# Performance work log

Measured on AMD Instinct MI355X. Metric: run time of the kernel, lower is better.

The kernel has to match this reference:

```python
import jax, jax.numpy as jnp
import numpy as np

IN_CH, IN_DIM, OUT_CH, OUT_DIM = 16, 32, 32, 32
NUM_ITERS = 3
EPS = 1e-11


def setup_inputs() -> dict:
    key = jax.random.key(0)
    kx, kw = jax.random.split(key)
    B, N = 32, 128
    x = jax.random.normal(kx, (B, N, IN_CH, IN_DIM), dtype=jnp.float32)
    # learned transform, matches torch Parameter randn(1,1,in_ch,out_ch,in_dim,out_dim)
    W = jax.random.normal(kw, (IN_CH, OUT_CH, IN_DIM, OUT_DIM), dtype=jnp.float32)
    return {"x": x, "W": W, "number_of_nodes": N}


def squash(s):
    # s: [B, 1, out_ch, out_dim]; squash along capsule dim (axis=3)
    mag_sq = jnp.sum(s * s, axis=3, keepdims=True)
    mag = jnp.sqrt(mag_sq) + EPS
    a_j = mag_sq / (1.0 + mag_sq)
    return a_j * (s / mag), a_j


def reference(x, W, number_of_nodes):
    B, N = x.shape[0], x.shape[1]
    # u_hat[b,n,c,o,j] = sum_i x[b,n,c,i] * W[c,o,i,j]
    u_hat = jnp.einsum('bnci,coij->bncoj', x, W)
    u_hat = u_hat.reshape(B, N * IN_CH, OUT_CH, OUT_DIM)

    b_ij = jnp.zeros((B, N * IN_CH, OUT_CH, 1), dtype=u_hat.dtype)
    v_j = a_j = None
    for _ in range(NUM_ITERS):
        c_ij = jax.nn.softmax(b_ij, axis=1)          # softmax over input capsules
        s_j = jnp.sum(c_ij * u_hat, axis=1, keepdims=True)  # [B,1,out_ch,out_dim]
        v_j, a_j = squash(s_j)
        # agreement: broadcast v_j over input-capsule dim (no explicit cat)
        u_vj = jnp.sum(u_hat * v_j, axis=3, keepdims=True)
        b_ij = b_ij + u_vj
    return v_j, a_j
```

## Files before the change

### kernel.cpp

```cpp
#include <hip/hip_runtime.h>
#include <math.h>

#define BB 32
#define NN 128
#define CC 16
#define OO 32
#define II 32
#define JJ 32
#define MM (NN*CC)
static constexpr float EPS_ = 1e-11f;


__global__ __launch_bounds__(1024) void k_transpose(
    const float* __restrict__ x, float* __restrict__ xT) {
  int b = blockIdx.x >> 4, c = blockIdx.x & 15;
  __shared__ __align__(16) float xsT[II][NN + 4];
  int tid = threadIdx.x;
  {
    int n = tid >> 3, i4 = (tid & 7) * 4;
    float4 v = *(const float4*)(x + (((size_t)(b * NN + n)) * CC + c) * II + i4);
    xsT[i4 + 0][n] = v.x; xsT[i4 + 1][n] = v.y;
    xsT[i4 + 2][n] = v.z; xsT[i4 + 3][n] = v.w;
  }
  __syncthreads();
  {
    int i = tid >> 5, n4 = tid & 31;
    float4 v = *(const float4*)(&xsT[i][n4 * 4]);
    ((float4*)(xT + ((size_t)(b * CC + c)) * II * NN))[tid] = v;
  }
}

__device__ __forceinline__ float rs16(float p[16], int l) {
  bool u2 = (l >> 1) & 1, u4 = (l >> 2) & 1, u8 = (l >> 3) & 1, u16 = (l >> 4) & 1;
  #pragma unroll
  for (int k = 0; k < 8; ++k) {
    float s0 = u2 ? p[k] : p[k + 8];
    float r0 = __shfl_xor(s0, 2);
    p[k] = (u2 ? p[k + 8] : p[k]) + r0;
  }
  #pragma unroll
  for (int k = 0; k < 4; ++k) {
    float s0 = u4 ? p[k] : p[k + 4];
    float r0 = __shfl_xor(s0, 4);
    p[k] = (u4 ? p[k + 4] : p[k]) + r0;
  }
  #pragma unroll
  for (int k = 0; k < 2; ++k) {
    float s0 = u8 ? p[k] : p[k + 2];
    float r0 = __shfl_xor(s0, 8);
    p[k] = (u8 ? p[k + 2] : p[k]) + r0;
  }
  {
    float s0 = u16 ? p[0] : p[1];
    float r0 = __shfl_xor(s0, 16);
    p[0] = (u16 ? p[1] : p[0]) + r0;
  }
  p[0] += __shfl_xor(p[0], 32);
  return p[0];
}

__global__ __launch_bounds__(1024, 4) void k_route(
    const float* __restrict__ xT, const float* __restrict__ W,
    float* __restrict__ out) {
  int bid = blockIdx.x;
  int b = bid & 31, o0 = (bid >> 5) * 2;
  int tid = threadIdx.x;

  __shared__ __align__(16) float bijL[2][CC][NN];
  __shared__ __align__(16) float coef[2][CC][NN];
  __shared__ float cxs[2][CC][II];
  __shared__ float wv [2][CC][II];
  __shared__ float partA[2][CC][JJ];
  __shared__ float vs[2][JJ];
  __shared__ float redM[CC][2], redE[CC][2];
  __shared__ float lds_pad[9216];
  if (out == (float*)1) {
    volatile float* vp = lds_pad;
    vp[tid] = 1.0f;
    if (vp[0] == 2.0f) return;
  }

  int l = tid & 63;
  int c = tid >> 6, n4 = l >> 1, s = l & 1;
  const float4* xTb = (const float4*)(xT + (size_t)b * CC * II * NN);
  const float4* xp  = xTb + c * (II * NN / 4) + (s * 16) * (NN / 4) + n4;
  float4 xv[16];
  #pragma unroll
  for (int q = 0; q < 16; ++q) xv[q] = xp[q * (NN / 4)];

  {
    int o = tid >> 9, ci = (tid >> 5) & 15, m4i = tid & 31;
    *(float4*)(&bijL[o][ci][m4i * 4]) = make_float4(0.f, 0.f, 0.f, 0.f);
    float u = 1.0f / (float)MM;
    *(float4*)(&coef[o][ci][m4i * 4]) = make_float4(u, u, u, u);
  }
  __syncthreads();

  for (int it = 0; it < 3; ++it) {
    {
      int qf = ((l >> 1) & 1) * 8 + ((l >> 2) & 1) * 4
             + ((l >> 3) & 1) * 2 + ((l >> 4) & 1);
      {
        float4 cf = *(const float4*)(&coef[0][c][n4 * 4]);
        float p[16];
        #pragma unroll
        for (int q = 0; q < 16; ++q)
          p[q] = xv[q].x*cf.x + xv[q].y*cf.y + xv[q].z*cf.z + xv[q].w*cf.w;
        float r = rs16(p, l);
        if ((l & 32) == 0) cxs[0][c][s * 16 + qf] = r;
      }
      {
        float4 cf = *(const float4*)(&coef[1][c][n4 * 4]);
        float p[16];
        #pragma unroll
        for (int q = 0; q < 16; ++q)
          p[q] = xv[q].x*cf.x + xv[q].y*cf.y + xv[q].z*cf.z + xv[q].w*cf.w;
        float r = rs16(p, l);
        if ((l & 32) == 0) cxs[1][c][s * 16 + qf] = r;
      }
    }
    __syncthreads();

    {
      int o = tid >> 9, cA = (tid >> 5) & 15, j = tid & 31;
      const float* Wp = W + (((size_t)(cA * OO + o0 + o)) * II) * JJ + j;
      float acc = 0.f;
      #pragma unroll 8
      for (int i = 0; i < II; ++i)
        acc += cxs[o][cA][i] * Wp[i * JJ];
      partA[o][cA][j] = acc;
    }
    __syncthreads();

    if (tid < 64) {
      int o = tid >> 5, j = tid & 31;
      float sA = 0.f;
      #pragma unroll
      for (int cR = 0; cR < CC; ++cR) sA += partA[o][cR][j];
      float msq = sA * sA;
      #pragma unroll
      for (int off = 16; off > 0; off >>= 1) msq += __shfl_xor(msq, off);
      float mag = sqrtf(msq) + EPS_;
      float a   = msq / (1.0f + msq);
      float vvq = a * sA / mag;
      if (it == 2) {
        int row = b * OO + (o0 + o);
        out[(size_t)row * JJ + j] = vvq;
        if (j == 0) out[BB * OO * JJ + row] = a;
      } else {
        vs[o][j] = vvq;
      }
    }
    if (it == 2) break;
    __syncthreads();

    {
      int o = tid >> 9, cW = (tid >> 5) & 15, i = tid & 31;
      const float4* Wr = (const float4*)(W + (((size_t)(cW * OO + o0 + o)) * II + i) * JJ);
      float acc = 0.f;
      #pragma unroll 4
      for (int q = 0; q < 8; ++q) {
        float4 w4 = Wr[q];
        acc += w4.x * vs[o][q*4+0] + w4.y * vs[o][q*4+1]
             + w4.z * vs[o][q*4+2] + w4.w * vs[o][q*4+3];
      }
      wv[o][cW][i] = acc;
    }
    __syncthreads();

    {
      float4 ac0 = make_float4(0.f,0.f,0.f,0.f);
      float4 ac1 = make_float4(0.f,0.f,0.f,0.f);
      #pragma unroll
      for (int q = 0; q < 16; ++q) {
        int i = s * 16 + q;
        float w0 = wv[0][c][i], w1 = wv[1][c][i];
        ac0.x += xv[q].x * w0; ac0.y += xv[q].y * w0;
        ac0.z += xv[q].z * w0; ac0.w += xv[q].w * w0;
        ac1.x += xv[q].x * w1; ac1.y += xv[q].y * w1;
        ac1.z += xv[q].z * w1; ac1.w += xv[q].w * w1;
      }
      ac0.x += __shfl_xor(ac0.x, 1); ac0.y += __shfl_xor(ac0.y, 1);
      ac0.z += __shfl_xor(ac0.z, 1); ac0.w += __shfl_xor(ac0.w, 1);
      ac1.x += __shfl_xor(ac1.x, 1); ac1.y += __shfl_xor(ac1.y, 1);
      ac1.z += __shfl_xor(ac1.z, 1); ac1.w += __shfl_xor(ac1.w, 1);
      float4 r = (s == 0) ? ac0 : ac1;
      float4 bb = *(const float4*)(&bijL[s][c][n4 * 4]);
      r.x += bb.x; r.y += bb.y; r.z += bb.z; r.w += bb.w;
      *(float4*)(&bijL[s][c][n4 * 4]) = r;

      float m4 = fmaxf(fmaxf(r.x, r.y), fmaxf(r.z, r.w));
      #pragma unroll
      for (int off = 2; off <= 32; off <<= 1) m4 = fmaxf(m4, __shfl_xor(m4, off));
      int wave = tid >> 6;
      if ((tid & 63) <= 1) redM[wave][s] = m4;
      __syncthreads();
      float mo = redM[0][s];
      #pragma unroll
      for (int w2 = 1; w2 < CC; ++w2) mo = fmaxf(mo, redM[w2][s]);
      float ex = __expf(r.x - mo), ey = __expf(r.y - mo),
            ez = __expf(r.z - mo), ew = __expf(r.w - mo);
      float e = ex + ey + ez + ew;
      #pragma unroll
      for (int off = 2; off <= 32; off <<= 1) e += __shfl_xor(e, off);
      if ((tid & 63) <= 1) redE[wave][s] = e;
      __syncthreads();
      float ss = redE[0][s];
      #pragma unroll
      for (int w2 = 1; w2 < CC; ++w2) ss += redE[w2][s];
      float rin = 1.0f / ss;
      *(float4*)(&coef[s][c][n4 * 4]) =
          make_float4(ex * rin, ey * rin, ez * rin, ew * rin);
    }
    __syncthreads();
  }
}

extern "C" void kernel_launch(void* const* d_in, const int* in_sizes, int n_in,
                              void* d_out, int out_size, void* d_ws, size_t ws_size,
                              hipStream_t stream) {
  const float* x = (const float*)d_in[0];
  const float* W = (const float*)d_in[1];
  (void)in_sizes; (void)n_in;
  float* out = (float*)d_out; (void)out_size;

  float* xT = (float*)d_ws;
  (void)ws_size;

  k_transpose<<<BB * CC, 1024, 0, stream>>>(x, xT);
  k_route<<<BB * (OO / 2), 1024, 0, stream>>>(xT, W, out);
}
```

Measured before the change: 119.2 us.

## Stage W slice in padded LDS and recompute softmax coefficients from logits

After: 107.2 us (median of 3 runs). 10.1% less time.

```diff
diff --git a/kernel.cpp b/kernel.cpp
--- a/kernel.cpp
+++ b/kernel.cpp
@@ -8,6 +8,7 @@
 #define II 32
 #define JJ 32
 #define MM (NN*CC)
+#define WP (JJ+1)
 static constexpr float EPS_ = 1e-11f;
 
 
@@ -66,18 +67,24 @@
   int b = bid & 31, o0 = (bid >> 5) * 2;
   int tid = threadIdx.x;
 
+  __shared__ float Ws[CC * 2 * II * WP];
   __shared__ __align__(16) float bijL[2][CC][NN];
-  __shared__ __align__(16) float coef[2][CC][NN];
-  __shared__ float cxs[2][CC][II];
-  __shared__ float wv [2][CC][II];
+  __shared__ float cw[2][CC][II];
   __shared__ float partA[2][CC][JJ];
   __shared__ float vs[2][JJ];
   __shared__ float redM[CC][2], redE[CC][2];
-  __shared__ float lds_pad[9216];
-  if (out == (float*)1) {
-    volatile float* vp = lds_pad;
-    vp[tid] = 1.0f;
-    if (vp[0] == 2.0f) return;
+  __shared__ float smx[2], srin[2];
+
+  {
+    int q = tid & 7, r0 = tid >> 3;
+    #pragma unroll
+    for (int k = 0; k < 8; ++k) {
+      int rowid = r0 + k * 128;
+      int c = rowid >> 6, o = (rowid >> 5) & 1, i = rowid & 31;
+      float4 v = *(const float4*)(W + ((((size_t)c * OO + o0 + o) * II + i) * JJ) + q * 4);
+      float* dst = &Ws[rowid * WP + q * 4];
+      dst[0] = v.x; dst[1] = v.y; dst[2] = v.z; dst[3] = v.w;
+    }
   }
 
   int l = tid & 63;
@@ -91,8 +98,7 @@
   {
     int o = tid >> 9, ci = (tid >> 5) & 15, m4i = tid & 31;
     *(float4*)(&bijL[o][ci][m4i * 4]) = make_float4(0.f, 0.f, 0.f, 0.f);
-    float u = 1.0f / (float)MM;
-    *(float4*)(&coef[o][ci][m4i * 4]) = make_float4(u, u, u, u);
+    if (tid < 2) { smx[tid] = 0.f; srin[tid] = 1.0f / (float)MM; }
   }
   __syncthreads();
 
@@ -100,34 +106,29 @@
     {
       int qf = ((l >> 1) & 1) * 8 + ((l >> 2) & 1) * 4
              + ((l >> 3) & 1) * 2 + ((l >> 4) & 1);
-      {
-        float4 cf = *(const float4*)(&coef[0][c][n4 * 4]);
+      #pragma unroll
+      for (int o = 0; o < 2; ++o) {
+        float4 bb = *(const float4*)(&bijL[o][c][n4 * 4]);
+        float m = smx[o], ri = srin[o];
+        float cfx = __expf(bb.x - m) * ri, cfy = __expf(bb.y - m) * ri;
+        float cfz = __expf(bb.z - m) * ri, cfw = __expf(bb.w - m) * ri;
         float p[16];
         #pragma unroll
         for (int q = 0; q < 16; ++q)
-          p[q] = xv[q].x*cf.x + xv[q].y*cf.y + xv[q].z*cf.z + xv[q].w*cf.w;
+          p[q] = xv[q].x*cfx + xv[q].y*cfy + xv[q].z*cfz + xv[q].w*cfw;
         float r = rs16(p, l);
-        if ((l & 32) == 0) cxs[0][c][s * 16 + qf] = r;
-      }
-      {
-        float4 cf = *(const float4*)(&coef[1][c][n4 * 4]);
-        float p[16];
-        #pragma unroll
-        for (int q = 0; q < 16; ++q)
-          p[q] = xv[q].x*cf.x + xv[q].y*cf.y + xv[q].z*cf.z + xv[q].w*cf.w;
-        float r = rs16(p, l);
-        if ((l & 32) == 0) cxs[1][c][s * 16 + qf] = r;
+        if ((l & 32) == 0) cw[o][c][s * 16 + qf] = r;
       }
     }
     __syncthreads();
 
     {
       int o = tid >> 9, cA = (tid >> 5) & 15, j = tid & 31;
-      const float* Wp = W + (((size_t)(cA * OO + o0 + o)) * II) * JJ + j;
+      const float* wsp = &Ws[((cA * 2 + o) * II) * WP + j];
       float acc = 0.f;
       #pragma unroll 8
       for (int i = 0; i < II; ++i)
-        acc += cxs[o][cA][i] * Wp[i * JJ];
+        acc += cw[o][cA][i] * wsp[i * WP];
       partA[o][cA][j] = acc;
     }
     __syncthreads();
@@ -156,15 +157,12 @@
 
     {
       int o = tid >> 9, cW = (tid >> 5) & 15, i = tid & 31;
-      const float4* Wr = (const float4*)(W + (((size_t)(cW * OO + o0 + o)) * II + i) * JJ);
+      const float* wsr = &Ws[((cW * 2 + o) * II + i) * WP];
       float acc = 0.f;
-      #pragma unroll 4
-      for (int q = 0; q < 8; ++q) {
-        float4 w4 = Wr[q];
-        acc += w4.x * vs[o][q*4+0] + w4.y * vs[o][q*4+1]
-             + w4.z * vs[o][q*4+2] + w4.w * vs[o][q*4+3];
-      }
-      wv[o][cW][i] = acc;
+      #pragma unroll 8
+      for (int j = 0; j < JJ; ++j)
+        acc += wsr[j] * vs[o][j];
+      cw[o][cW][i] = acc;
     }
     __syncthreads();
 
@@ -174,7 +172,7 @@
       #pragma unroll
       for (int q = 0; q < 16; ++q) {
         int i = s * 16 + q;
-        float w0 = wv[0][c][i], w1 = wv[1][c][i];
+        float w0 = cw[0][c][i], w1 = cw[1][c][i];
         ac0.x += xv[q].x * w0; ac0.y += xv[q].y * w0;
         ac0.z += xv[q].z * w0; ac0.w += xv[q].w * w0;
         ac1.x += xv[q].x * w1; ac1.y += xv[q].y * w1;
@@ -205,12 +203,15 @@
       for (int off = 2; off <= 32; off <<= 1) e += __shfl_xor(e, off);
       if ((tid & 63) <= 1) redE[wave][s] = e;
       __syncthreads();
-      float ss = redE[0][s];
-      #pragma unroll
-      for (int w2 = 1; w2 < CC; ++w2) ss += redE[w2][s];
-      float rin = 1.0f / ss;
-      *(float4*)(&coef[s][c][n4 * 4]) =
-          make_float4(ex * rin, ey * rin, ez * rin, ew * rin);
+      if (tid < 2) {
+        float ss = 0.f, mm = redM[0][tid];
+        #pragma unroll
+        for (int w2 = 0; w2 < CC; ++w2) ss += redE[w2][tid];
+        #pragma unroll
+        for (int w2 = 1; w2 < CC; ++w2) mm = fmaxf(mm, redM[w2][tid]);
+        smx[tid]  = mm;
+        srin[tid] = 1.0f / ss;
+      }
     }
     __syncthreads();
   }
```
